# Optimization experiments

Measured on AMD Instinct MI355X. Metric: run time of the kernel, lower is better.

Reference implementation:

```python
import jax, jax.numpy as jnp
import numpy as np

NBITS = 4
QN, QP = -(2 ** (NBITS - 1)), 2 ** (NBITS - 1) - 1  # -8, 7
NUM_HEADS = 12


def round_ste(x):
    # round_pass: straight-through estimator round
    return x + jax.lax.stop_gradient(jnp.round(x) - x)


def act3b(x, alpha, bias=0.0, signed=True):
    qn, qp = (-4.0, 3.0) if signed else (0.0, 7.0)
    return round_ste(jnp.clip((x + bias) / alpha, qn, qp))


def setup_inputs() -> dict:
    key = jax.random.key(0)
    ks = jax.random.split(key, 20)
    B, N, C, H = 32, 512, 768, NUM_HEADS
    hd = C // H
    u = lambda k, s: jax.random.uniform(k, s, jnp.float32, 0.05, 0.15)
    return {
        'x0': jax.random.normal(ks[0], (B, N, C), jnp.float32),
        'qkv_w': 0.02 * jax.random.normal(ks[1], (3 * C, C), jnp.float32),
        'qkv_alpha': u(ks[2], (3 * C,)),
        'qkv_bias': 0.02 * jax.random.normal(ks[3], (3 * C,), jnp.float32),
        'qkv_act_alpha': u(ks[4], (C,)),
        'proj_w': 0.02 * jax.random.normal(ks[5], (C, C), jnp.float32),
        'proj_alpha': u(ks[6], (C,)),
        'proj_bias': 0.02 * jax.random.normal(ks[7], (C,), jnp.float32),
        'proj_act_alpha': u(ks[8], (C,)),
        'normq_w': jax.random.uniform(ks[9], (hd,), jnp.float32, 0.8, 1.2),
        'normq_b': 0.01 * jax.random.normal(ks[10], (hd,), jnp.float32),
        'normk_w': jax.random.uniform(ks[11], (hd,), jnp.float32, 0.8, 1.2),
        'normk_b': 0.01 * jax.random.normal(ks[12], (hd,), jnp.float32),
        'qact_alpha': u(ks[13], (H,)),
        'kact_alpha': u(ks[14], (H,)),
        'vact_alpha': u(ks[15], (H,)),
        'attnact_alpha': u(ks[16], (H,)),
    }


def reference(x0, qkv_w, qkv_alpha, qkv_bias, qkv_act_alpha, proj_w, proj_alpha,
              proj_bias, proj_act_alpha, normq_w, normq_b, normk_w, normk_b,
              qact_alpha, kact_alpha, vact_alpha, attnact_alpha):
    B, N, C = x0.shape
    H = NUM_HEADS
    hd = C // H
    scale = hd ** -0.5

    # input activation quant (ActQ_v2, nbits=4)
    a_in = qkv_act_alpha.mean()
    x0_q = round_ste(jnp.clip(x0 / a_in, QN, QP))
    # kernel-wise 4-bit weight quant for qkv (no dequant here; scales folded later)
    w_q = round_ste(jnp.clip(qkv_w / qkv_alpha[:, None], QN, QP))
    qkv = x0_q @ w_q.T
    # integer-domain bias (truncated toward zero, like .int())
    qkv = qkv + jnp.trunc(qkv_bias / a_in / qkv_alpha)

    qkv = qkv.reshape(B, N, 3, H, hd).transpose(2, 0, 3, 1, 4)  # [3,B,H,N,hd]
    q0, k0, v0 = qkv[0], qkv[1], qkv[2]
    alpha3 = qkv_alpha.reshape(3, H, 1, hd)

    # fused scaled LayerNorm + 3-bit quant for q and k
    def norm_quant(x, ch_scale, nw, nb, act_a):
        xs = x * ch_scale  # [B,H,N,hd]
        centered = xs - xs.mean(-1, keepdims=True)
        std = jnp.std(xs, axis=-1, ddof=1, keepdims=True)
        return act3b(centered / (std + 1e-5), alpha=act_a / nw, bias=nb / nw)

    q2 = norm_quant(q0, alpha3[0], normq_w, normq_b, qact_alpha.mean())
    k2 = norm_quant(k0, alpha3[1], normk_w, normk_b, kact_alpha.mean())
    v2 = act3b(v0, alpha=vact_alpha.mean() / (a_in * alpha3[2]))

    # integer QK^T
    qk = jnp.einsum('bhqd,bhkd->bhqk', q2, k2)

    # base-2 softmax approximation
    div = 128.0
    sm_scale = scale * qact_alpha.mean() * kact_alpha.mean()
    e = jnp.trunc((1.0 / np.log(2)) * sm_scale * qk * div)
    attn_exp = jnp.exp2(jnp.round(e / div))
    attn = act3b(attn_exp / attn_exp.sum(-1, keepdims=True),
                 alpha=attnact_alpha.mean(), signed=False)

    # integer AV
    x1 = jnp.einsum('bhqk,bhkd->bhqd', attn, v2)
    x1 = x1.transpose(0, 2, 1, 3).reshape(B, N, C)
    x1_q = act3b(x1, alpha=proj_act_alpha.mean() / (attnact_alpha.mean() * vact_alpha.mean()))

    pw_q = round_ste(jnp.clip(proj_w / proj_alpha[:, None], QN, QP))
    out = (x1_q @ pw_q.T) * proj_alpha * proj_act_alpha.mean() + proj_bias
    return out
```

## Files before the change

kernel.cpp:

```cpp
#include <hip/hip_runtime.h>
#include <stdint.h>


#define BB 32
#define NN 512
#define CC 768
#define HH 12
#define HD 64
#define M_ROWS (BB * NN)
#define QKV_C (3 * CC)
#define KTA ((size_t)M_ROWS * 64)
#define KTB ((size_t)QKV_C * 64)
#define KTP ((size_t)CC * 64)

typedef int v4i __attribute__((ext_vector_type(4)));
typedef int v16i __attribute__((ext_vector_type(16)));

__device__ __forceinline__ float fadd(float a, float b) { return __fadd_rn(a, b); }
__device__ __forceinline__ float fmul(float a, float b) { return __fmul_rn(a, b); }
__device__ __forceinline__ float fdiv(float a, float b) { return __fdiv_rn(a, b); }
__device__ __forceinline__ float fsub(float a, float b) { return __fsub_rn(a, b); }

__device__ float np_sum_96(const float* a) {
  float r[8];
#pragma unroll
  for (int j = 0; j < 8; j++) r[j] = a[j];
  for (int i = 8; i < 96; i += 8)
#pragma unroll
    for (int j = 0; j < 8; j++) r[j] = fadd(r[j], a[i + j]);
  return fadd(fadd(fadd(r[0], r[1]), fadd(r[2], r[3])),
              fadd(fadd(r[4], r[5]), fadd(r[6], r[7])));
}

__device__ float np_mean_12(const float* a) {
  float r[8];
#pragma unroll
  for (int j = 0; j < 8; j++) r[j] = a[j];
  float res = fadd(fadd(fadd(r[0], r[1]), fadd(r[2], r[3])),
                   fadd(fadd(r[4], r[5]), fadd(r[6], r[7])));
  res = fadd(res, a[8]);
  res = fadd(res, a[9]);
  res = fadd(res, a[10]);
  res = fadd(res, a[11]);
  return fdiv(res, 12.0f);
}

__global__ void prep_kernel(const float* __restrict__ qkv_act_alpha,
                            const float* __restrict__ proj_act_alpha,
                            const float* __restrict__ qact_alpha,
                            const float* __restrict__ kact_alpha,
                            const float* __restrict__ vact_alpha,
                            const float* __restrict__ attnact_alpha,
                            const float* __restrict__ normq_w,
                            const float* __restrict__ normq_b,
                            const float* __restrict__ normk_w,
                            const float* __restrict__ normk_b,
                            const float* __restrict__ qkv_bias,
                            const float* __restrict__ qkv_alpha,
                            float* __restrict__ scal,
                            float* __restrict__ qparams,
                            float* __restrict__ biasq) {
  __shared__ float s_scal[8];
  __shared__ float chunk[16];
  int tid = threadIdx.x;
  if (tid < 8) chunk[tid] = np_sum_96(qkv_act_alpha + 96 * tid);
  else if (tid < 16) chunk[tid] = np_sum_96(proj_act_alpha + 96 * (tid - 8));
  if (tid == 16) s_scal[1] = np_mean_12(qact_alpha);
  if (tid == 17) s_scal[2] = np_mean_12(kact_alpha);
  if (tid == 18) s_scal[3] = np_mean_12(vact_alpha);
  if (tid == 19) s_scal[4] = np_mean_12(attnact_alpha);
  __syncthreads();
  if (tid == 0) {
    float s0 = fadd(fadd(chunk[0], chunk[1]), fadd(chunk[2], chunk[3]));
    float s1 = fadd(fadd(chunk[4], chunk[5]), fadd(chunk[6], chunk[7]));
    s_scal[0] = fdiv(fadd(s0, s1), 768.0f);
    float p0 = fadd(fadd(chunk[8], chunk[9]), fadd(chunk[10], chunk[11]));
    float p1 = fadd(fadd(chunk[12], chunk[13]), fadd(chunk[14], chunk[15]));
    s_scal[5] = fdiv(fadd(p0, p1), 768.0f);
  }
  __syncthreads();
  if (tid < 6) scal[tid] = s_scal[tid];
  if (tid < 64) {
    qparams[tid]       = fdiv(s_scal[1], normq_w[tid]);
    qparams[64 + tid]  = fdiv(normq_b[tid], normq_w[tid]);
    qparams[128 + tid] = fdiv(s_scal[2], normk_w[tid]);
    qparams[192 + tid] = fdiv(normk_b[tid], normk_w[tid]);
  }
  float a_in = s_scal[0];
  for (int c = tid; c < QKV_C; c += blockDim.x)
    biasq[c] = truncf(fdiv(fdiv(qkv_bias[c], a_in), qkv_alpha[c]));
}

__device__ __forceinline__ size_t fragaddr(int row, int b) {
  return (size_t)(row & ~31) * 64 + ((b >> 4) * 512 + (row & 31) * 16 + (b & 15));
}

__global__ void quant_x0_kernel(const float* __restrict__ x0,
                                const float* __restrict__ scal,
                                int8_t* __restrict__ x0q, int total4) {
  int i = blockIdx.x * blockDim.x + threadIdx.x;
  if (i >= total4) return;
  float a_in = scal[0];
  float4 v = ((const float4*)x0)[i];
  char4 o;
  o.x = (int8_t)rintf(fminf(fmaxf(fdiv(v.x, a_in), -8.f), 7.f));
  o.y = (int8_t)rintf(fminf(fmaxf(fdiv(v.y, a_in), -8.f), 7.f));
  o.z = (int8_t)rintf(fminf(fmaxf(fdiv(v.z, a_in), -8.f), 7.f));
  o.w = (int8_t)rintf(fminf(fmaxf(fdiv(v.w, a_in), -8.f), 7.f));
  int seq = i / 192;
  int kp = (i - seq * 192) * 4;
  int b = kp & 63;
  *(char4*)(x0q + (size_t)(kp >> 6) * KTA + fragaddr(seq, b)) = o;
}

__global__ void quant_w_kernel(const float* __restrict__ w,
                               const float* __restrict__ alpha,
                               int8_t* __restrict__ wq, int rows, int total) {
  int i = blockIdx.x * blockDim.x + threadIdx.x;
  if (i >= total) return;
  int row = i / CC;
  int k = i - row * CC;
  float t = fminf(fmaxf(fdiv(w[i], alpha[row]), -8.f), 7.f);
  wq[(size_t)(k >> 6) * ((size_t)rows * 64) + fragaddr(row, k)] =
      (int8_t)rintf(t);
}

__global__ __launch_bounds__(256) void gemm_qkv_kernel(
    const int8_t* __restrict__ Aq, const int8_t* __restrict__ Wq,
    const float* __restrict__ biasq, const float* __restrict__ scal,
    const float* __restrict__ qkv_alpha, const float* __restrict__ qparams,
    int8_t* __restrict__ q2, int8_t* __restrict__ k2,
    int8_t* __restrict__ v2f) {
  __shared__ __align__(16) int8_t packT[4][3072];

  const int L = blockIdx.x;
  const int xcd = L & 7, s = L >> 3;
  const int rb = xcd + 8 * (s / 36);
  const int g = s % 36;
  const int tid = threadIdx.x;
  const int w = tid >> 6, lane = tid & 63;
  const int l31 = lane & 31, hi = lane >> 5;
  const int sec = g / HH, head = g % HH;
  const int col0 = g * 64;
  const int b_idx = rb >> 1, nbase = (rb & 1) * 256;
  const int w64 = w * 64;
  const size_t bh = (size_t)b_idx * HH + head;

  v16i acc00 = (v16i)(0), acc01 = (v16i)(0);
  v16i acc10 = (v16i)(0), acc11 = (v16i)(0);

  const int8_t* pa = Aq + (size_t)(rb * 256 + w64) * 64 + hi * 512 + l31 * 16;
  const int8_t* pb = Wq + (size_t)col0 * 64 + hi * 512 + l31 * 16;

  if (sec < 2) {
    v4i A0a = *(const v4i*)(pa);
    v4i A0b = *(const v4i*)(pa + 1024);
    v4i A1a = *(const v4i*)(pa + 2048);
    v4i A1b = *(const v4i*)(pa + 3072);
#pragma unroll 1
    for (int kt = 0; kt < 11; kt++) {
      const int8_t* pbk = pb + (size_t)kt * KTB;
      v4i B0a = *(const v4i*)(pbk);
      v4i B0b = *(const v4i*)(pbk + 1024);
      v4i B1a = *(const v4i*)(pbk + 2048);
      v4i B1b = *(const v4i*)(pbk + 3072);
      const int8_t* npa = pa + (size_t)(kt + 1) * KTA;
      v4i nA0a = *(const v4i*)(npa);
      v4i nA0b = *(const v4i*)(npa + 1024);
      v4i nA1a = *(const v4i*)(npa + 2048);
      v4i nA1b = *(const v4i*)(npa + 3072);
      acc00 = __builtin_amdgcn_mfma_i32_32x32x32_i8(B0a, A0a, acc00, 0, 0, 0);
      acc01 = __builtin_amdgcn_mfma_i32_32x32x32_i8(B1a, A0a, acc01, 0, 0, 0);
      acc10 = __builtin_amdgcn_mfma_i32_32x32x32_i8(B0a, A1a, acc10, 0, 0, 0);
      acc11 = __builtin_amdgcn_mfma_i32_32x32x32_i8(B1a, A1a, acc11, 0, 0, 0);
      acc00 = __builtin_amdgcn_mfma_i32_32x32x32_i8(B0b, A0b, acc00, 0, 0, 0);
      acc01 = __builtin_amdgcn_mfma_i32_32x32x32_i8(B1b, A0b, acc01, 0, 0, 0);
      acc10 = __builtin_amdgcn_mfma_i32_32x32x32_i8(B0b, A1b, acc10, 0, 0, 0);
      acc11 = __builtin_amdgcn_mfma_i32_32x32x32_i8(B1b, A1b, acc11, 0, 0, 0);
      A0a = nA0a; A0b = nA0b; A1a = nA1a; A1b = nA1b;
    }
    {
      const int8_t* pbk = pb + (size_t)11 * KTB;
      v4i B0a = *(const v4i*)(pbk);
      v4i B0b = *(const v4i*)(pbk + 1024);
      v4i B1a = *(const v4i*)(pbk + 2048);
      v4i B1b = *(const v4i*)(pbk + 3072);
      acc00 = __builtin_amdgcn_mfma_i32_32x32x32_i8(B0a, A0a, acc00, 0, 0, 0);
      acc01 = __builtin_amdgcn_mfma_i32_32x32x32_i8(B1a, A0a, acc01, 0, 0, 0);
      acc10 = __builtin_amdgcn_mfma_i32_32x32x32_i8(B0a, A1a, acc10, 0, 0, 0);
      acc11 = __builtin_amdgcn_mfma_i32_32x32x32_i8(B1a, A1a, acc11, 0, 0, 0);
      acc00 = __builtin_amdgcn_mfma_i32_32x32x32_i8(B0b, A0b, acc00, 0, 0, 0);
      acc01 = __builtin_amdgcn_mfma_i32_32x32x32_i8(B1b, A0b, acc01, 0, 0, 0);
      acc10 = __builtin_amdgcn_mfma_i32_32x32x32_i8(B0b, A1b, acc10, 0, 0, 0);
      acc11 = __builtin_amdgcn_mfma_i32_32x32x32_i8(B1b, A1b, acc11, 0, 0, 0);
    }

    const float* ap = qparams + (sec == 0 ? 0 : 128);
    int8_t* dst = (sec == 0) ? q2 : k2;
#pragma unroll
    for (int p = 0; p < 2; p++) {
      float xs[2][16];
#pragma unroll
      for (int i = 0; i < 2; i++)
#pragma unroll
        for (int b = 0; b < 4; b++) {
          int cg = col0 + 32 * i + 8 * b + 4 * hi;
          float4 bqv = *(const float4*)(biasq + cg);
          float4 alv = *(const float4*)(qkv_alpha + cg);
          const float* bqp = (const float*)&bqv;
          const float* alp = (const float*)&alv;
#pragma unroll
          for (int c = 0; c < 4; c++) {
            int av;
            if (p == 0)
              av = (i == 0) ? acc00[4 * b + c] : acc01[4 * b + c];
            else
              av = (i == 0) ? acc10[4 * b + c] : acc11[4 * b + c];
            xs[i][4 * b + c] = fmul(fadd((float)av, bqp[c]), alp[c]);
          }
        }
      float rc[4];
#pragma unroll
      for (int c = 0; c < 4; c++) rc[c] = xs[0][c];
#pragma unroll
      for (int b = 1; b < 4; b++)
#pragma unroll
        for (int c = 0; c < 4; c++) rc[c] = fadd(rc[c], xs[0][4 * b + c]);
#pragma unroll
      for (int b = 0; b < 4; b++)
#pragma unroll
        for (int c = 0; c < 4; c++) rc[c] = fadd(rc[c], xs[1][4 * b + c]);
      float Ls = fadd(fadd(rc[0], rc[1]), fadd(rc[2], rc[3]));
      float Rs = __shfl_xor(Ls, 32, 64);
      float mn = fdiv(fadd(Ls, Rs), 64.0f);
      float vc[4];
#pragma unroll
      for (int c = 0; c < 4; c++) {
        float d = fsub(xs[0][c], mn);
        vc[c] = fmul(d, d);
      }
#pragma unroll
      for (int b = 1; b < 4; b++)
#pragma unroll
        for (int c = 0; c < 4; c++) {
          float d = fsub(xs[0][4 * b + c], mn);
          vc[c] = fadd(vc[c], fmul(d, d));
        }
#pragma unroll
      for (int b = 0; b < 4; b++)
#pragma unroll
        for (int c = 0; c < 4; c++) {
          float d = fsub(xs[1][4 * b + c], mn);
          vc[c] = fadd(vc[c], fmul(d, d));
        }
      float Lv = fadd(fadd(vc[0], vc[1]), fadd(vc[2], vc[3]));
      float Rv = __shfl_xor(Lv, 32, 64);
      float var = fdiv(fadd(Lv, Rv), 63.0f);
      float den = fadd(__fsqrt_rn(var), 1e-5f);
#pragma unroll
      for (int i = 0; i < 2; i++)
#pragma unroll
        for (int b = 0; b < 4; b++) {
          int cin = 32 * i + 8 * b + 4 * hi;
          float4 a4 = *(const float4*)(ap + cin);
          float4 b4 = *(const float4*)(ap + 64 + cin);
          const float* a4p = (const float*)&a4;
          const float* b4p = (const float*)&b4;
          uint32_t pk = 0;
#pragma unroll
          for (int c = 0; c < 4; c++) {
            float xn = fdiv(fsub(xs[i][4 * b + c], mn), den);
            float t = fdiv(fadd(xn, b4p[c]), a4p[c]);
            t = fminf(fmaxf(t, -4.f), 3.f);
            pk |= ((uint32_t)(uint8_t)(int8_t)rintf(t)) << (8 * c);
          }
          *(uint32_t*)&packT[w][l31 * 80 + cin] = pk;
        }
      asm volatile("s_waitcnt lgkmcnt(0)" ::: "memory");
      size_t rowbase = bh * NN + nbase + w64 + p * 32;
#pragma unroll
      for (int c = 0; c < 2; c++) {
        int id = lane + 64 * c;
        int row = id >> 2, off = (id & 3) * 16;
        int4 ov = *(const int4*)&packT[w][row * 80 + off];
        *(int4*)(dst + (rowbase + row) * 64 + off) = ov;
      }
    }
  } else {
    v4i A0a = *(const v4i*)(pa);
    v4i A0b = *(const v4i*)(pa + 1024);
    v4i A1a = *(const v4i*)(pa + 2048);
    v4i A1b = *(const v4i*)(pa + 3072);
#pragma unroll 1
    for (int kt = 0; kt < 11; kt++) {
      const int8_t* pbk = pb + (size_t)kt * KTB;
      v4i B0a = *(const v4i*)(pbk);
      v4i B0b = *(const v4i*)(pbk + 1024);
      v4i B1a = *(const v4i*)(pbk + 2048);
      v4i B1b = *(const v4i*)(pbk + 3072);
      const int8_t* npa = pa + (size_t)(kt + 1) * KTA;
      v4i nA0a = *(const v4i*)(npa);
      v4i nA0b = *(const v4i*)(npa + 1024);
      v4i nA1a = *(const v4i*)(npa + 2048);
      v4i nA1b = *(const v4i*)(npa + 3072);
      acc00 = __builtin_amdgcn_mfma_i32_32x32x32_i8(A0a, B0a, acc00, 0, 0, 0);
      acc01 = __builtin_amdgcn_mfma_i32_32x32x32_i8(A0a, B1a, acc01, 0, 0, 0);
      acc10 = __builtin_amdgcn_mfma_i32_32x32x32_i8(A1a, B0a, acc10, 0, 0, 0);
      acc11 = __builtin_amdgcn_mfma_i32_32x32x32_i8(A1a, B1a, acc11, 0, 0, 0);
      acc00 = __builtin_amdgcn_mfma_i32_32x32x32_i8(A0b, B0b, acc00, 0, 0, 0);
      acc01 = __builtin_amdgcn_mfma_i32_32x32x32_i8(A0b, B1b, acc01, 0, 0, 0);
      acc10 = __builtin_amdgcn_mfma_i32_32x32x32_i8(A1b, B0b, acc10, 0, 0, 0);
      acc11 = __builtin_amdgcn_mfma_i32_32x32x32_i8(A1b, B1b, acc11, 0, 0, 0);
      A0a = nA0a; A0b = nA0b; A1a = nA1a; A1b = nA1b;
    }
    {
      const int8_t* pbk = pb + (size_t)11 * KTB;
      v4i B0a = *(const v4i*)(pbk);
      v4i B0b = *(const v4i*)(pbk + 1024);
      v4i B1a = *(const v4i*)(pbk + 2048);
      v4i B1b = *(const v4i*)(pbk + 3072);
      acc00 = __builtin_amdgcn_mfma_i32_32x32x32_i8(A0a, B0a, acc00, 0, 0, 0);
      acc01 = __builtin_amdgcn_mfma_i32_32x32x32_i8(A0a, B1a, acc01, 0, 0, 0);
      acc10 = __builtin_amdgcn_mfma_i32_32x32x32_i8(A1a, B0a, acc10, 0, 0, 0);
      acc11 = __builtin_amdgcn_mfma_i32_32x32x32_i8(A1a, B1a, acc11, 0, 0, 0);
      acc00 = __builtin_amdgcn_mfma_i32_32x32x32_i8(A0b, B0b, acc00, 0, 0, 0);
      acc01 = __builtin_amdgcn_mfma_i32_32x32x32_i8(A0b, B1b, acc01, 0, 0, 0);
      acc10 = __builtin_amdgcn_mfma_i32_32x32x32_i8(A1b, B0b, acc10, 0, 0, 0);
      acc11 = __builtin_amdgcn_mfma_i32_32x32x32_i8(A1b, B1b, acc11, 0, 0, 0);
    }

    const float a_in = scal[0], vact = scal[3];
#pragma unroll
    for (int p = 0; p < 2; p++) {
#pragma unroll
      for (int sj = 0; sj < 2; sj++) {
        int cg = col0 + 32 * sj + l31;
        float bq = biasq[cg];
        float va = fdiv(vact, fmul(a_in, qkv_alpha[cg]));
        int dloc = 32 * sj + l31;
#pragma unroll
        for (int b = 0; b < 4; b++) {
          uint32_t pk = 0;
#pragma unroll
          for (int c = 0; c < 4; c++) {
            int av;
            if (p == 0)
              av = (sj == 0) ? acc00[4 * b + c] : acc01[4 * b + c];
            else
              av = (sj == 0) ? acc10[4 * b + c] : acc11[4 * b + c];
            float vint = fadd((float)av, bq);
            float t = fminf(fmaxf(fdiv(vint, va), -4.f), 3.f);
            pk |= ((uint32_t)(uint8_t)(int8_t)rintf(t)) << (8 * c);
          }
          *(uint32_t*)&packT[w][dloc * 48 + 8 * b + 4 * hi] = pk;
        }
      }
      asm volatile("s_waitcnt lgkmcnt(0)" ::: "memory");
#pragma unroll
      for (int c = 0; c < 2; c++) {
        int id = lane + 64 * c;
        int row = id >> 1, off = (id & 1) * 16;
        int4 ov = *(const int4*)&packT[w][row * 48 + off];
        int n0 = nbase + w64 + p * 32 + off;
        *(int4*)(v2f + (size_t)bh * 32768 + ((n0 >> 6) * 4096) +
                 ((row >> 4) * 1024) + ((row & 15) * 64) +
                 (((n0 >> 4) & 3) * 16)) = ov;
      }
    }
  }
}

__global__ __launch_bounds__(256) void attn_kernel(
    const int8_t* __restrict__ q2, const int8_t* __restrict__ k2,
    const int8_t* __restrict__ v2f, const float* __restrict__ scal,
    int8_t* __restrict__ x1q) {
  __shared__ __align__(16) int8_t At[64][80];
  __shared__ __align__(16) uint32_t mpL[4096];

  const int L = blockIdx.x;
  const int xcd = L & 7, s = L >> 3;
  const int bh = xcd + 8 * (s >> 3);
  const int qt = s & 7;
  const int tid = threadIdx.x;
  const int w = tid >> 6, lane = tid & 63, quad = lane >> 4, c16 = lane & 15;
  const int sr = tid >> 2, scol = (tid & 3) << 4;
  const float attnm = scal[4];
  const float coef =
      fmul(1.4426950408889634f, fmul(fmul(0.125f, scal[1]), scal[2]));
  const float coef128 = fmul(coef, 128.f);
  const size_t base = (size_t)bh * NN * HD;
  const int mpbase = w * 1024 + lane * 4;

  const int8_t* kptr = k2 + base + (size_t)c16 * 64 + quad * 16;
  const int8_t* vptr = v2f + base + (size_t)c16 * 64 + quad * 16;
  v4i qf = *(const v4i*)(q2 + base + (size_t)(qt * 64 + 16 * w + c16) * 64 +
                         quad * 16);

  uint32_t mpack[4][4];
  float Srow = 0.f;
  v4i kfr[2];
  kfr[0] = *(const v4i*)(kptr);
  kfr[1] = *(const v4i*)(kptr + 1024);
#pragma unroll
  for (int kt = 0; kt < 8; kt++) {
    float psum = 0.f;
    uint32_t mp[4];
#pragma unroll
    for (int f = 0; f < 4; f++) {
      int p = kt * 4 + f;
      v4i kf = kfr[p & 1];
      if (p + 2 < 32) kfr[p & 1] = *(const v4i*)(kptr + (p + 2) * 1024);
      v4i d2 = (v4i){0, 0, 0, 0};
      d2 = __builtin_amdgcn_mfma_i32_16x16x64_i8(kf, qf, d2, 0, 0, 0);
      uint32_t pk = 0;
#pragma unroll
      for (int r = 0; r < 4; r++) {
        float e = truncf(fmul(coef128, (float)d2[r]));
        int mi = (int)rintf(fmul(e, 0.0078125f));
        psum = fadd(psum, ldexpf(1.0f, mi));
        pk |= ((uint32_t)(uint8_t)(int8_t)mi) << (8 * r);
      }
      mp[f] = pk;
    }
    if (kt < 4) {
#pragma unroll
      for (int f = 0; f < 4; f++) mpack[kt][f] = mp[f];
    } else {
      int4 st;
      st.x = (int)mp[0]; st.y = (int)mp[1]; st.z = (int)mp[2]; st.w = (int)mp[3];
      *(int4*)&mpL[mpbase + (kt - 4) * 256] = st;
    }
    psum = fadd(psum, __shfl_xor(psum, 16, 64));
    psum = fadd(psum, __shfl_xor(psum, 32, 64));
    Srow = fadd(Srow, psum);
  }
  const float u = fdiv(fdiv(1.0f, Srow), attnm);

  v4i xacc[4];
#pragma unroll
  for (int s2 = 0; s2 < 4; s2++) xacc[s2] = (v4i){0, 0, 0, 0};
  v4i vfr[4];
#pragma unroll
  for (int s2 = 0; s2 < 4; s2++)
    vfr[s2] = *(const v4i*)(vptr + s2 * 1024);

#pragma unroll
  for (int kt = 0; kt < 8; kt++) {
    uint32_t mp[4];
    if (kt < 4) {
#pragma unroll
      for (int f = 0; f < 4; f++) mp[f] = mpack[kt][f];
    } else {
      int4 ld = *(const int4*)&mpL[mpbase + (kt - 4) * 256];
      mp[0] = (uint32_t)ld.x; mp[1] = (uint32_t)ld.y;
      mp[2] = (uint32_t)ld.z; mp[3] = (uint32_t)ld.w;
    }
#pragma unroll
    for (int f = 0; f < 4; f++) {
      uint32_t pk = mp[f];
      uint32_t wpk = 0;
#pragma unroll
      for (int r = 0; r < 4; r++) {
        int mi = (int)(int8_t)(pk >> (8 * r));
        float t = fminf(ldexpf(u, mi), 7.f);
        wpk |= ((uint32_t)(uint8_t)(int8_t)rintf(t)) << (8 * r);
      }
      *(uint32_t*)&At[16 * w + c16][16 * f + 4 * quad] = wpk;
    }
    asm volatile("s_waitcnt lgkmcnt(0)" ::: "memory");
    v4i af = *(const v4i*)&At[16 * w + c16][quad * 16];
#pragma unroll
    for (int s2 = 0; s2 < 4; s2++) {
      v4i vf = vfr[s2];
      if (kt < 7)
        vfr[s2] = *(const v4i*)(vptr + (kt + 1) * 4096 + s2 * 1024);
      xacc[s2] = __builtin_amdgcn_mfma_i32_16x16x64_i8(vf, af, xacc[s2], 0, 0, 0);
    }
  }

  const float pa = fdiv(scal[5], fmul(attnm, scal[3]));
#pragma unroll
  for (int s2 = 0; s2 < 4; s2++) {
    uint32_t pack = 0;
#pragma unroll
    for (int r = 0; r < 4; r++) {
      float t = fminf(fmaxf(fdiv((float)xacc[s2][r], pa), -4.f), 3.f);
      pack |= ((uint32_t)(uint8_t)(int8_t)rintf(t)) << (8 * r);
    }
    *(uint32_t*)&At[16 * w + c16][16 * s2 + 4 * quad] = pack;
  }
  __syncthreads();
  int4 ov = *(const int4*)&At[sr][scol];
  *(int4*)(x1q + ((size_t)bh * NN + qt * 64 + sr) * HD + scol) = ov;
}

__global__ __launch_bounds__(256) void gemm_proj_kernel(
    const int8_t* __restrict__ x1q, const int8_t* __restrict__ Wq,
    const float* __restrict__ proj_alpha, const float* __restrict__ proj_bias,
    const float* __restrict__ scal, float* __restrict__ out) {
  const int L = blockIdx.x;
  const int xcd = L & 7, s = L >> 3;
  const int rb = xcd + 8 * (s / 12);
  const int g = s % 12;
  const int tid = threadIdx.x;
  const int w = tid >> 6, lane = tid & 63;
  const int l31 = lane & 31, hi = lane >> 5;
  const int col0 = g * 64;
  const int b_idx = rb >> 1, nbase = (rb & 1) * 256;
  const int w64 = w * 64;

  v16i acc00 = (v16i)(0), acc01 = (v16i)(0);
  v16i acc10 = (v16i)(0), acc11 = (v16i)(0);

  const int8_t* pa =
      x1q + ((size_t)b_idx * HH * NN + nbase + w64 + l31) * 64 + hi * 16;
  const int8_t* pb = Wq + (size_t)col0 * 64 + hi * 512 + l31 * 16;
  const size_t KTX = (size_t)NN * 64;

  v4i A0a = *(const v4i*)(pa);
  v4i A0b = *(const v4i*)(pa + 32);
  v4i A1a = *(const v4i*)(pa + 2048);
  v4i A1b = *(const v4i*)(pa + 2048 + 32);
#pragma unroll 1
  for (int kt = 0; kt < 11; kt++) {
    const int8_t* pbk = pb + (size_t)kt * KTP;
    v4i B0a = *(const v4i*)(pbk);
    v4i B0b = *(const v4i*)(pbk + 1024);
    v4i B1a = *(const v4i*)(pbk + 2048);
    v4i B1b = *(const v4i*)(pbk + 3072);
    const int8_t* npa = pa + (size_t)(kt + 1) * KTX;
    v4i nA0a = *(const v4i*)(npa);
    v4i nA0b = *(const v4i*)(npa + 32);
    v4i nA1a = *(const v4i*)(npa + 2048);
    v4i nA1b = *(const v4i*)(npa + 2048 + 32);
    acc00 = __builtin_amdgcn_mfma_i32_32x32x32_i8(B0a, A0a, acc00, 0, 0, 0);
    acc01 = __builtin_amdgcn_mfma_i32_32x32x32_i8(B1a, A0a, acc01, 0, 0, 0);
    acc10 = __builtin_amdgcn_mfma_i32_32x32x32_i8(B0a, A1a, acc10, 0, 0, 0);
    acc11 = __builtin_amdgcn_mfma_i32_32x32x32_i8(B1a, A1a, acc11, 0, 0, 0);
    acc00 = __builtin_amdgcn_mfma_i32_32x32x32_i8(B0b, A0b, acc00, 0, 0, 0);
    acc01 = __builtin_amdgcn_mfma_i32_32x32x32_i8(B1b, A0b, acc01, 0, 0, 0);
    acc10 = __builtin_amdgcn_mfma_i32_32x32x32_i8(B0b, A1b, acc10, 0, 0, 0);
    acc11 = __builtin_amdgcn_mfma_i32_32x32x32_i8(B1b, A1b, acc11, 0, 0, 0);
    A0a = nA0a; A0b = nA0b; A1a = nA1a; A1b = nA1b;
  }
  {
    const int8_t* pbk = pb + (size_t)11 * KTP;
    v4i B0a = *(const v4i*)(pbk);
    v4i B0b = *(const v4i*)(pbk + 1024);
    v4i B1a = *(const v4i*)(pbk + 2048);
    v4i B1b = *(const v4i*)(pbk + 3072);
    acc00 = __builtin_amdgcn_mfma_i32_32x32x32_i8(B0a, A0a, acc00, 0, 0, 0);
    acc01 = __builtin_amdgcn_mfma_i32_32x32x32_i8(B1a, A0a, acc01, 0, 0, 0);
    acc10 = __builtin_amdgcn_mfma_i32_32x32x32_i8(B0a, A1a, acc10, 0, 0, 0);
    acc11 = __builtin_amdgcn_mfma_i32_32x32x32_i8(B1a, A1a, acc11, 0, 0, 0);
    acc00 = __builtin_amdgcn_mfma_i32_32x32x32_i8(B0b, A0b, acc00, 0, 0, 0);
    acc01 = __builtin_amdgcn_mfma_i32_32x32x32_i8(B1b, A0b, acc01, 0, 0, 0);
    acc10 = __builtin_amdgcn_mfma_i32_32x32x32_i8(B0b, A1b, acc10, 0, 0, 0);
    acc11 = __builtin_amdgcn_mfma_i32_32x32x32_i8(B1b, A1b, acc11, 0, 0, 0);
  }

  const float pact = scal[5];
#pragma unroll
  for (int p = 0; p < 2; p++) {
    const int m = rb * 256 + w64 + p * 32 + l31;
#pragma unroll
    for (int i = 0; i < 2; i++)
#pragma unroll
      for (int b = 0; b < 4; b++) {
        int colb = col0 + 32 * i + 8 * b + 4 * hi;
        float4 al = *(const float4*)(proj_alpha + colb);
        float4 bi = *(const float4*)(proj_bias + colb);
        const float* alp = (const float*)&al;
        const float* bip = (const float*)&bi;
        float4 o;
        float* op = (float*)&o;
#pragma unroll
        for (int c = 0; c < 4; c++) {
          int av;
          if (p == 0)
            av = (i == 0) ? acc00[4 * b + c] : acc01[4 * b + c];
          else
            av = (i == 0) ? acc10[4 * b + c] : acc11[4 * b + c];
          op[c] = fadd(fmul(fmul((float)av, alp[c]), pact), bip[c]);
        }
        *(float4*)(out + (size_t)m * CC + colb) = o;
      }
  }
}

extern "C" void kernel_launch(void* const* d_in, const int* in_sizes, int n_in,
                              void* d_out, int out_size, void* d_ws,
                              size_t ws_size, hipStream_t stream) {
  const float* x0 = (const float*)d_in[0];
  const float* qkv_w = (const float*)d_in[1];
  const float* qkv_alpha = (const float*)d_in[2];
  const float* qkv_bias = (const float*)d_in[3];
  const float* qkv_act_alpha = (const float*)d_in[4];
  const float* proj_w = (const float*)d_in[5];
  const float* proj_alpha = (const float*)d_in[6];
  const float* proj_bias = (const float*)d_in[7];
  const float* proj_act_alpha = (const float*)d_in[8];
  const float* normq_w = (const float*)d_in[9];
  const float* normq_b = (const float*)d_in[10];
  const float* normk_w = (const float*)d_in[11];
  const float* normk_b = (const float*)d_in[12];
  const float* qact_alpha = (const float*)d_in[13];
  const float* kact_alpha = (const float*)d_in[14];
  const float* vact_alpha = (const float*)d_in[15];
  const float* attnact_alpha = (const float*)d_in[16];

  char* ws = (char*)d_ws;
  size_t off = 0;
  auto alloc = [&](size_t bytes) -> char* {
    char* p = ws + off;
    off += (bytes + 255) & ~(size_t)255;
    return p;
  };
  float* scal = (float*)alloc(64 * 4);
  float* qparams = (float*)alloc(256 * 4);
  float* biasq = (float*)alloc(QKV_C * 4);
  int8_t* x0q = (int8_t*)alloc((size_t)M_ROWS * CC);
  int8_t* wq = (int8_t*)alloc((size_t)QKV_C * CC);
  int8_t* pwq = (int8_t*)alloc((size_t)CC * CC);
  int8_t* q2 = (int8_t*)alloc((size_t)BB * HH * NN * HD);
  int8_t* k2 = (int8_t*)alloc((size_t)BB * HH * NN * HD);
  int8_t* v2f = (int8_t*)alloc((size_t)BB * HH * NN * HD);
  int8_t* x1q = (int8_t*)alloc((size_t)M_ROWS * CC);

  prep_kernel<<<1, 256, 0, stream>>>(qkv_act_alpha, proj_act_alpha, qact_alpha,
                                     kact_alpha, vact_alpha, attnact_alpha,
                                     normq_w, normq_b, normk_w, normk_b,
                                     qkv_bias, qkv_alpha, scal, qparams, biasq);

  int total4 = M_ROWS * CC / 4;
  quant_x0_kernel<<<(total4 + 255) / 256, 256, 0, stream>>>(x0, scal, x0q,
                                                            total4);
  quant_w_kernel<<<(QKV_C * CC + 255) / 256, 256, 0, stream>>>(
      qkv_w, qkv_alpha, wq, QKV_C, QKV_C * CC);
  quant_w_kernel<<<(CC * CC + 255) / 256, 256, 0, stream>>>(
      proj_w, proj_alpha, pwq, CC, CC * CC);

  gemm_qkv_kernel<<<36 * (M_ROWS / 256), 256, 0, stream>>>(
      x0q, wq, biasq, scal, qkv_alpha, qparams, q2, k2, v2f);

  attn_kernel<<<(NN / 64) * (BB * HH), 256, 0, stream>>>(q2, k2, v2f, scal,
                                                         x1q);

  gemm_proj_kernel<<<12 * (M_ROWS / 256), 256, 0, stream>>>(
      x1q, pwq, proj_alpha, proj_bias, scal, (float*)d_out);
}
```

Measured before the change: 283.4 us.

## Stage QKV GEMM operands through double-buffered LDS via async global_load_lds

```diff
diff --git a/kernel.cpp b/kernel.cpp
--- a/kernel.cpp
+++ b/kernel.cpp
@@ -20,6 +20,12 @@
 __device__ __forceinline__ float fmul(float a, float b) { return __fmul_rn(a, b); }
 __device__ __forceinline__ float fdiv(float a, float b) { return __fdiv_rn(a, b); }
 __device__ __forceinline__ float fsub(float a, float b) { return __fsub_rn(a, b); }
+
+__device__ __forceinline__ void gload_lds16(const int8_t* g, int8_t* l) {
+  __builtin_amdgcn_global_load_lds(
+      (const __attribute__((address_space(1))) void*)g,
+      (__attribute__((address_space(3))) void*)l, 16, 0, 0);
+}
 
 __device__ float np_sum_96(const float* a) {
   float r[8];
@@ -131,6 +137,8 @@
     const float* __restrict__ qkv_alpha, const float* __restrict__ qparams,
     int8_t* __restrict__ q2, int8_t* __restrict__ k2,
     int8_t* __restrict__ v2f) {
+  __shared__ __align__(16) int8_t sA[2][16384];
+  __shared__ __align__(16) int8_t sB[2][4096];
   __shared__ __align__(16) int8_t packT[4][3072];
 
   const int L = blockIdx.x;
@@ -149,26 +157,40 @@
   v16i acc00 = (v16i)(0), acc01 = (v16i)(0);
   v16i acc10 = (v16i)(0), acc11 = (v16i)(0);
 
-  const int8_t* pa = Aq + (size_t)(rb * 256 + w64) * 64 + hi * 512 + l31 * 16;
-  const int8_t* pb = Wq + (size_t)col0 * 64 + hi * 512 + l31 * 16;
-
-  if (sec < 2) {
-    v4i A0a = *(const v4i*)(pa);
-    v4i A0b = *(const v4i*)(pa + 1024);
-    v4i A1a = *(const v4i*)(pa + 2048);
-    v4i A1b = *(const v4i*)(pa + 3072);
+  const int8_t* Ag = Aq + (size_t)(rb * 256) * 64;
+  const int8_t* Bg = Wq + (size_t)col0 * 64;
+  const int t16 = tid * 16;
+  const int foff = hi * 512 + l31 * 16;
+  const bool qk = (sec < 2);
+
+  {
+    const int8_t* ga = Ag + t16;
+#pragma unroll
+    for (int i = 0; i < 4; i++)
+      gload_lds16(ga + i * 4096, &sA[0][i * 4096 + t16]);
+    gload_lds16(Bg + t16, &sB[0][t16]);
+  }
+  __syncthreads();
+
 #pragma unroll 1
-    for (int kt = 0; kt < 11; kt++) {
-      const int8_t* pbk = pb + (size_t)kt * KTB;
-      v4i B0a = *(const v4i*)(pbk);
-      v4i B0b = *(const v4i*)(pbk + 1024);
-      v4i B1a = *(const v4i*)(pbk + 2048);
-      v4i B1b = *(const v4i*)(pbk + 3072);
-      const int8_t* npa = pa + (size_t)(kt + 1) * KTA;
-      v4i nA0a = *(const v4i*)(npa);
-      v4i nA0b = *(const v4i*)(npa + 1024);
-      v4i nA1a = *(const v4i*)(npa + 2048);
-      v4i nA1b = *(const v4i*)(npa + 3072);
+  for (int kt = 0; kt < 12; kt++) {
+    const int cur = kt & 1;
+    if (kt < 11) {
+      const int8_t* ga = Ag + (size_t)(kt + 1) * KTA + t16;
+#pragma unroll
+      for (int i = 0; i < 4; i++)
+        gload_lds16(ga + i * 4096, &sA[cur ^ 1][i * 4096 + t16]);
+      gload_lds16(Bg + (size_t)(kt + 1) * KTB + t16, &sB[cur ^ 1][t16]);
+    }
+    v4i A0a = *(const v4i*)&sA[cur][w * 4096 + foff];
+    v4i A0b = *(const v4i*)&sA[cur][w * 4096 + foff + 1024];
+    v4i A1a = *(const v4i*)&sA[cur][w * 4096 + foff + 2048];
+    v4i A1b = *(const v4i*)&sA[cur][w * 4096 + foff + 3072];
+    v4i B0a = *(const v4i*)&sB[cur][foff];
+    v4i B0b = *(const v4i*)&sB[cur][foff + 1024];
+    v4i B1a = *(const v4i*)&sB[cur][foff + 2048];
+    v4i B1b = *(const v4i*)&sB[cur][foff + 3072];
+    if (qk) {
       acc00 = __builtin_amdgcn_mfma_i32_32x32x32_i8(B0a, A0a, acc00, 0, 0, 0);
       acc01 = __builtin_amdgcn_mfma_i32_32x32x32_i8(B1a, A0a, acc01, 0, 0, 0);
       acc10 = __builtin_amdgcn_mfma_i32_32x32x32_i8(B0a, A1a, acc10, 0, 0, 0);
@@ -177,24 +199,20 @@
       acc01 = __builtin_amdgcn_mfma_i32_32x32x32_i8(B1b, A0b, acc01, 0, 0, 0);
       acc10 = __builtin_amdgcn_mfma_i32_32x32x32_i8(B0b, A1b, acc10, 0, 0, 0);
       acc11 = __builtin_amdgcn_mfma_i32_32x32x32_i8(B1b, A1b, acc11, 0, 0, 0);
-      A0a = nA0a; A0b = nA0b; A1a = nA1a; A1b = nA1b;
-    }
-    {
-      const int8_t* pbk = pb + (size_t)11 * KTB;
-      v4i B0a = *(const v4i*)(pbk);
-      v4i B0b = *(const v4i*)(pbk + 1024);
-      v4i B1a = *(const v4i*)(pbk + 2048);
-      v4i B1b = *(const v4i*)(pbk + 3072);
-      acc00 = __builtin_amdgcn_mfma_i32_32x32x32_i8(B0a, A0a, acc00, 0, 0, 0);
-      acc01 = __builtin_amdgcn_mfma_i32_32x32x32_i8(B1a, A0a, acc01, 0, 0, 0);
-      acc10 = __builtin_amdgcn_mfma_i32_32x32x32_i8(B0a, A1a, acc10, 0, 0, 0);
-      acc11 = __builtin_amdgcn_mfma_i32_32x32x32_i8(B1a, A1a, acc11, 0, 0, 0);
-      acc00 = __builtin_amdgcn_mfma_i32_32x32x32_i8(B0b, A0b, acc00, 0, 0, 0);
-      acc01 = __builtin_amdgcn_mfma_i32_32x32x32_i8(B1b, A0b, acc01, 0, 0, 0);
-      acc10 = __builtin_amdgcn_mfma_i32_32x32x32_i8(B0b, A1b, acc10, 0, 0, 0);
-      acc11 = __builtin_amdgcn_mfma_i32_32x32x32_i8(B1b, A1b, acc11, 0, 0, 0);
-    }
-
+    } else {
+      acc00 = __builtin_amdgcn_mfma_i32_32x32x32_i8(A0a, B0a, acc00, 0, 0, 0);
+      acc01 = __builtin_amdgcn_mfma_i32_32x32x32_i8(A0a, B1a, acc01, 0, 0, 0);
+      acc10 = __builtin_amdgcn_mfma_i32_32x32x32_i8(A1a, B0a, acc10, 0, 0, 0);
+      acc11 = __builtin_amdgcn_mfma_i32_32x32x32_i8(A1a, B1a, acc11, 0, 0, 0);
+      acc00 = __builtin_amdgcn_mfma_i32_32x32x32_i8(A0b, B0b, acc00, 0, 0, 0);
+      acc01 = __builtin_amdgcn_mfma_i32_32x32x32_i8(A0b, B1b, acc01, 0, 0, 0);
+      acc10 = __builtin_amdgcn_mfma_i32_32x32x32_i8(A1b, B0b, acc10, 0, 0, 0);
+      acc11 = __builtin_amdgcn_mfma_i32_32x32x32_i8(A1b, B1b, acc11, 0, 0, 0);
+    }
+    __syncthreads();
+  }
+
+  if (qk) {
     const float* ap = qparams + (sec == 0 ? 0 : 128);
     int8_t* dst = (sec == 0) ? q2 : k2;
 #pragma unroll
@@ -287,48 +305,6 @@
       }
     }
   } else {
-    v4i A0a = *(const v4i*)(pa);
-    v4i A0b = *(const v4i*)(pa + 1024);
-    v4i A1a = *(const v4i*)(pa + 2048);
-    v4i A1b = *(const v4i*)(pa + 3072);
-#pragma unroll 1
-    for (int kt = 0; kt < 11; kt++) {
-      const int8_t* pbk = pb + (size_t)kt * KTB;
-      v4i B0a = *(const v4i*)(pbk);
-      v4i B0b = *(const v4i*)(pbk + 1024);
-      v4i B1a = *(const v4i*)(pbk + 2048);
-      v4i B1b = *(const v4i*)(pbk + 3072);
-      const int8_t* npa = pa + (size_t)(kt + 1) * KTA;
-      v4i nA0a = *(const v4i*)(npa);
-      v4i nA0b = *(const v4i*)(npa + 1024);
-      v4i nA1a = *(const v4i*)(npa + 2048);
-      v4i nA1b = *(const v4i*)(npa + 3072);
-      acc00 = __builtin_amdgcn_mfma_i32_32x32x32_i8(A0a, B0a, acc00, 0, 0, 0);
-      acc01 = __builtin_amdgcn_mfma_i32_32x32x32_i8(A0a, B1a, acc01, 0, 0, 0);
-      acc10 = __builtin_amdgcn_mfma_i32_32x32x32_i8(A1a, B0a, acc10, 0, 0, 0);
-      acc11 = __builtin_amdgcn_mfma_i32_32x32x32_i8(A1a, B1a, acc11, 0, 0, 0);
-      acc00 = __builtin_amdgcn_mfma_i32_32x32x32_i8(A0b, B0b, acc00, 0, 0, 0);
-      acc01 = __builtin_amdgcn_mfma_i32_32x32x32_i8(A0b, B1b, acc01, 0, 0, 0);
-      acc10 = __builtin_amdgcn_mfma_i32_32x32x32_i8(A1b, B0b, acc10, 0, 0, 0);
-      acc11 = __builtin_amdgcn_mfma_i32_32x32x32_i8(A1b, B1b, acc11, 0, 0, 0);
-      A0a = nA0a; A0b = nA0b; A1a = nA1a; A1b = nA1b;
-    }
-    {
-      const int8_t* pbk = pb + (size_t)11 * KTB;
-      v4i B0a = *(const v4i*)(pbk);
-      v4i B0b = *(const v4i*)(pbk + 1024);
-      v4i B1a = *(const v4i*)(pbk + 2048);
-      v4i B1b = *(const v4i*)(pbk + 3072);
-      acc00 = __builtin_amdgcn_mfma_i32_32x32x32_i8(A0a, B0a, acc00, 0, 0, 0);
-      acc01 = __builtin_amdgcn_mfma_i32_32x32x32_i8(A0a, B1a, acc01, 0, 0, 0);
-      acc10 = __builtin_amdgcn_mfma_i32_32x32x32_i8(A1a, B0a, acc10, 0, 0, 0);
-      acc11 = __builtin_amdgcn_mfma_i32_32x32x32_i8(A1a, B1a, acc11, 0, 0, 0);
-      acc00 = __builtin_amdgcn_mfma_i32_32x32x32_i8(A0b, B0b, acc00, 0, 0, 0);
-      acc01 = __builtin_amdgcn_mfma_i32_32x32x32_i8(A0b, B1b, acc01, 0, 0, 0);
-      acc10 = __builtin_amdgcn_mfma_i32_32x32x32_i8(A1b, B0b, acc10, 0, 0, 0);
-      acc11 = __builtin_amdgcn_mfma_i32_32x32x32_i8(A1b, B1b, acc11, 0, 0, 0);
-    }
-
     const float a_in = scal[0], vact = scal[3];
 #pragma unroll
     for (int p = 0; p < 2; p++) {
```

Result: slower. 359.8 us (+27.0%).
